# Optimization experiments

Measured on AMD Instinct MI355X. Metric: run time of the kernel, lower is better.

## Reference

```python
import jax, jax.numpy as jnp
import numpy as np

B, T, V, E, H = 4096, 16, 512, 512, 1024


def setup_inputs() -> dict:
    key = jax.random.key(0)
    ks = jax.random.split(key, 8)
    s = 0.05  # weight init scale
    return {
        "encoded_input": jax.random.normal(ks[0], (B, H), jnp.float32),
        "target": jax.random.randint(ks[1], (B, T), 0, V, jnp.int32),
        "emb": jax.random.normal(ks[2], (V, E), jnp.float32) * s,
        "W_ih": jax.random.normal(ks[3], (4 * H, E), jnp.float32) * s,
        "W_hh": jax.random.normal(ks[4], (4 * H, H), jnp.float32) * s,
        "b_ih": jax.random.normal(ks[5], (4 * H,), jnp.float32) * s,
        "b_hh": jax.random.normal(ks[6], (4 * H,), jnp.float32) * s,
        "W_out": jax.random.normal(ks[7], (V, H), jnp.float32) * s,
    }


def reference(encoded_input, target, emb, W_ih, W_hh, b_ih, b_hh, W_out):
    # Teacher-forced char LSTM decoder. Dropout(0.1) is identity in eval mode.
    b, t = target.shape
    # input char ids: start token 0, then shifted targets
    inp_ids = jnp.concatenate(
        [jnp.zeros((b, 1), target.dtype), target[:, :-1]], axis=1)  # [B,T]
    x = emb[inp_ids]  # [B,T,E]
    # precompute input contribution to gates for all steps
    xg = jnp.einsum('bte,ge->btg', x, W_ih) + b_ih + b_hh  # [B,T,4H]

    def step(carry, xs):
        h, c = carry
        xg_t, tgt_t = xs  # [B,4H], [B]
        gates = xg_t + h @ W_hh.T  # [B,4H]
        i, f, g, o = jnp.split(gates, 4, axis=-1)  # torch order i,f,g,o
        i = jax.nn.sigmoid(i)
        f = jax.nn.sigmoid(f)
        g = jnp.tanh(g)
        o = jax.nn.sigmoid(o)
        c = f * c + i * g
        h = o * jnp.tanh(c)
        logits = h @ W_out.T  # [B,V]
        # NLL of log_softmax at target index, expressed stably
        lse = jax.nn.logsumexp(logits, axis=-1)
        tgt_logit = jnp.take_along_axis(logits, tgt_t[:, None], axis=1)[:, 0]
        loss_t = lse - tgt_logit  # [B]
        return (h, c), loss_t

    h0 = encoded_input  # hidden = (encoded, encoded) for 1 layer
    (_, _), losses = jax.lax.scan(
        step, (h0, h0),
        (jnp.swapaxes(xg, 0, 1), target.T))  # scan over time: [T,B,...]
    return losses.sum(axis=0) / t  # [B] per-example mean loss
```

## Files before the change

### kernel.cpp

```cpp
#include <hip/hip_runtime.h>
#include <hip/hip_bf16.h>
#include <stdint.h>

typedef __attribute__((ext_vector_type(8))) short bf16x8;
typedef __attribute__((ext_vector_type(4))) float f32x4;

#define DEV __device__ __forceinline__
#define MFMA16(a, b, c) __builtin_amdgcn_mfma_f32_16x16x32_bf16(a, b, c, 0, 0, 0)

static constexpr int Bn = 4096;
static constexpr int Tn = 16;
static constexpr int Vn = 512;
static constexpr int En = 512;
static constexpr int Hn = 1024;
static constexpr int G4 = 4096;

DEV unsigned short f2bf(float f) {
    union { float f; uint32_t u; } v; v.f = f;
    return (unsigned short)((v.u + 0x7fffu + ((v.u >> 16) & 1u)) >> 16);
}
DEV float bf2f(unsigned short h) {
    union { uint32_t u; float f; } v; v.u = (uint32_t)h << 16; return v.f;
}
DEV float sigmoidf_(float x) { return 1.f / (1.f + __expf(-x)); }
DEV float tanhf_(float x)    { return 1.f - 2.f / (1.f + __expf(2.f * x)); }

DEV bf16x8 cvt8(const float* p) {
    f32x4 a = *(const f32x4*)p;
    f32x4 b = *(const f32x4*)(p + 4);
    bf16x8 o;
    o[0] = (short)f2bf(a[0]); o[1] = (short)f2bf(a[1]);
    o[2] = (short)f2bf(a[2]); o[3] = (short)f2bf(a[3]);
    o[4] = (short)f2bf(b[0]); o[5] = (short)f2bf(b[1]);
    o[6] = (short)f2bf(b[2]); o[7] = (short)f2bf(b[3]);
    return o;
}

#define GLOAD16(s, d) __builtin_amdgcn_global_load_lds( \
    (const __attribute__((address_space(1))) uint32_t*)(s), \
    (__attribute__((address_space(3))) uint32_t*)(d), 16, 0, 0)

__launch_bounds__(512, 2)
__global__ void lstm8(const unsigned short* __restrict__ Whp8,
                      const unsigned short* __restrict__ Hin,
                      const float* __restrict__ EGb,
                      const int* __restrict__ target, int t,
                      float* __restrict__ CstF,
                      unsigned short* __restrict__ Hout)
{
    __shared__ __align__(16) unsigned short lds[65536];

    const int tid = threadIdx.x;
    const int l   = tid & 63;
    const int w   = tid >> 6;
    const int wm  = w >> 2, wn = w & 3;
    const int q   = l >> 4, c15 = l & 15;
    const int bx  = blockIdx.x, by = blockIdx.y;
    const int n0  = bx * 256;

    const int cB    = (((l & 7) ^ (l >> 3)) << 3);
    const int sw0   = ((q ^ (c15 & 7)) << 3);
    const int offA0 = c15 * 64 + sw0;
    const int offB0 = ((wn & 1) * 64 + c15) * 64 + sw0;

    f32x4 acc[8][4];
#pragma unroll
    for (int i = 0; i < 8; i++)
#pragma unroll
        for (int j = 0; j < 4; j++) acc[i][j] = f32x4{0.f, 0.f, 0.f, 0.f};

    auto stA = [&](int kts, int cbuf) {
        const unsigned short* page =
            Whp8 + (((size_t)(by * 16 + kts) * 2) << 13);
#pragma unroll
        for (int h = 0; h < 2; h++)
#pragma unroll
            for (int L = 0; L < 2; L++)
                GLOAD16(page + h * 8192 + L * 4096 + w * 512 + l * 8,
                        &lds[cbuf * 16384 + h * 8192 + L * 4096 + w * 512]);
    };
    auto stB = [&](int kts, int cbuf) {
#pragma unroll
        for (int h = 0; h < 2; h++)
#pragma unroll
            for (int L = 0; L < 2; L++)
                GLOAD16(Hin + (size_t)(n0 + h * 128 + L * 64 + w * 8 + (l >> 3)) * Hn
                            + kts * 64 + cB,
                        &lds[32768 + cbuf * 16384 + h * 8192 + L * 4096 + w * 512]);
    };

    stA(0, 0); stB(0, 0);
    stA(1, 1); stB(1, 1);
    asm volatile("s_waitcnt vmcnt(8)" ::: "memory");
    __builtin_amdgcn_s_barrier();

#pragma unroll 2
    for (int kt = 0; kt < 16; kt++) {
        const int cur = kt & 1;
        const unsigned short* Ab = &lds[cur * 16384 + wm * 8192];
        const unsigned short* Bb = &lds[32768 + cur * 16384 + (wn >> 1) * 8192];
        bf16x8 aF[8], bF[4];

#pragma unroll
        for (int i = 0; i < 8; i++)
            aF[i] = *(const bf16x8*)&Ab[offA0 + i * 1024];
#pragma unroll
        for (int j = 0; j < 4; j++)
            bF[j] = *(const bf16x8*)&Bb[offB0 + j * 1024];
        __builtin_amdgcn_s_setprio(1);
#pragma unroll
        for (int i = 0; i < 8; i++)
#pragma unroll
            for (int j = 0; j < 4; j++)
                acc[i][j] = MFMA16(aF[i], bF[j], acc[i][j]);
        __builtin_amdgcn_s_setprio(0);

#pragma unroll
        for (int i = 0; i < 8; i++)
            aF[i] = *(const bf16x8*)&Ab[(offA0 ^ 32) + i * 1024];
#pragma unroll
        for (int j = 0; j < 4; j++)
            bF[j] = *(const bf16x8*)&Bb[(offB0 ^ 32) + j * 1024];
        __builtin_amdgcn_s_setprio(1);
#pragma unroll
        for (int i = 0; i < 8; i++)
#pragma unroll
            for (int j = 0; j < 4; j++)
                acc[i][j] = MFMA16(aF[i], bF[j], acc[i][j]);
        __builtin_amdgcn_s_setprio(0);
        __builtin_amdgcn_s_barrier();

        const int kts = (kt + 2 < 16) ? (kt + 2) : 15;
        stA(kts, cur);
        stB(kts, cur);
        asm volatile("s_waitcnt vmcnt(8)" ::: "memory");
        __builtin_amdgcn_s_barrier();
    }

    int ids[4];
#pragma unroll
    for (int j = 0; j < 4; j++)
        ids[j] = (t > 0)
            ? target[(size_t)(n0 + wn * 64 + j * 16 + c15) * Tn + (t - 1)] : 0;

    const int U0 = by * 64;
    unsigned short* sH = &lds[32768];
#pragma unroll
    for (int i = 0; i < 8; i++) {
        const int Uloc = wm * 32 + i * 4 + q;
#pragma unroll
        for (int j = 0; j < 4; j++) {
            f32x4 eg = *(const f32x4*)&EGb[(size_t)ids[j] * G4 + (U0 + Uloc) * 4];
            float ig = sigmoidf_(acc[i][j][0] + eg[0]);
            float fg = sigmoidf_(acc[i][j][1] + eg[1]);
            float gg = tanhf_  (acc[i][j][2] + eg[2]);
            float og = sigmoidf_(acc[i][j][3] + eg[3]);
            const size_t cidx =
                ((((size_t)(by * 16 + bx) * 8 + w) * 32 + i * 4 + j) << 6) + l;
            float cOld = CstF[cidx];
            float cNew = fg * cOld + ig * gg;
            float h    = og * tanhf_(cNew);
            CstF[cidx] = cNew;
            const int bl = wn * 64 + j * 16 + c15;
            sH[bl * 64 + (Uloc ^ ((bl & 7) << 3))] = f2bf(h);
        }
    }
    __syncthreads();
    {
        const int row = tid >> 1;
        const int hs  = tid & 1;
        const int sx  = row & 7;
        size_t go = (size_t)(n0 + row) * Hn + U0 + hs * 32;
#pragma unroll
        for (int s = 0; s < 4; s++) {
            const int slog = hs * 4 + s;
            bf16x8 v = *(const bf16x8*)&sH[row * 64 + ((slog ^ sx) << 3)];
            *(bf16x8*)&Hout[go + s * 8] = v;
        }
    }
}

__launch_bounds__(512, 1)
__global__ void logits256(const unsigned short* __restrict__ A,
                          const unsigned short* __restrict__ Wob,
                          const int* __restrict__ target,
                          float* __restrict__ partS,
                          float* __restrict__ partT)
{
    __shared__ __align__(16) unsigned short lds[65536];
    __shared__ float redS[4 * 256];
    __shared__ float redT[4 * 256];
    __shared__ int   tgL[256];

    const int tid = threadIdx.x;
    const int l   = tid & 63;
    const int w   = tid >> 6;
    const int wm  = w >> 2, wn = w & 3;
    const int q   = l >> 4, c15 = l & 15;
    const int bid = blockIdx.x;
    const int rb  = bid & 255, cb = bid >> 8;
    const int r0  = rb * 256;
    const int v0  = cb * 256;

    if (tid < 256) {
        int ra = r0 + tid;
        tgL[tid] = target[(size_t)(ra & (Bn - 1)) * Tn + (ra >> 12)];
    }

    const int cB    = (((l & 7) ^ (l >> 3)) << 3);
    const int sw0   = ((q ^ (c15 & 7)) << 3);
    const int offA0 = c15 * 64 + sw0;
    const int offB0 = ((wn & 1) * 64 + c15) * 64 + sw0;

    f32x4 acc[8][4];
#pragma unroll
    for (int i = 0; i < 8; i++)
#pragma unroll
        for (int j = 0; j < 4; j++) acc[i][j] = f32x4{0.f, 0.f, 0.f, 0.f};

    auto stA = [&](int kts, int cbuf) {
#pragma unroll
        for (int h = 0; h < 2; h++)
#pragma unroll
            for (int L = 0; L < 2; L++)
                GLOAD16(A + (size_t)(r0 + h * 128 + L * 64 + w * 8 + (l >> 3)) * Hn
                            + kts * 64 + cB,
                        &lds[cbuf * 16384 + h * 8192 + L * 4096 + w * 512]);
    };
    auto stB = [&](int kts, int cbuf) {
#pragma unroll
        for (int h = 0; h < 2; h++)
#pragma unroll
            for (int L = 0; L < 2; L++)
                GLOAD16(Wob + (size_t)(v0 + h * 128 + L * 64 + w * 8 + (l >> 3)) * Hn
                            + kts * 64 + cB,
                        &lds[32768 + cbuf * 16384 + h * 8192 + L * 4096 + w * 512]);
    };

    stA(0, 0); stB(0, 0);
    stA(1, 1); stB(1, 1);
    asm volatile("s_waitcnt vmcnt(8)" ::: "memory");
    __builtin_amdgcn_s_barrier();

#pragma unroll 2
    for (int kt = 0; kt < 16; kt++) {
        const int cur = kt & 1;
        const unsigned short* Ab = &lds[cur * 16384 + wm * 8192];
        const unsigned short* Bb = &lds[32768 + cur * 16384 + (wn >> 1) * 8192];
        bf16x8 aF[8], bF[4];

#pragma unroll
        for (int i = 0; i < 8; i++)
            aF[i] = *(const bf16x8*)&Ab[offA0 + i * 1024];
#pragma unroll
        for (int j = 0; j < 4; j++)
            bF[j] = *(const bf16x8*)&Bb[offB0 + j * 1024];
        __builtin_amdgcn_s_setprio(1);
#pragma unroll
        for (int i = 0; i < 8; i++)
#pragma unroll
            for (int j = 0; j < 4; j++)
                acc[i][j] = MFMA16(aF[i], bF[j], acc[i][j]);
        __builtin_amdgcn_s_setprio(0);

#pragma unroll
        for (int i = 0; i < 8; i++)
            aF[i] = *(const bf16x8*)&Ab[(offA0 ^ 32) + i * 1024];
#pragma unroll
        for (int j = 0; j < 4; j++)
            bF[j] = *(const bf16x8*)&Bb[(offB0 ^ 32) + j * 1024];
        __builtin_amdgcn_s_setprio(1);
#pragma unroll
        for (int i = 0; i < 8; i++)
#pragma unroll
            for (int j = 0; j < 4; j++)
                acc[i][j] = MFMA16(aF[i], bF[j], acc[i][j]);
        __builtin_amdgcn_s_setprio(0);
        __builtin_amdgcn_s_barrier();

        const int kts = (kt + 2 < 16) ? (kt + 2) : 15;
        stA(kts, cur);
        stB(kts, cur);
        asm volatile("s_waitcnt vmcnt(8)" ::: "memory");
        __builtin_amdgcn_s_barrier();
    }

#pragma unroll
    for (int i = 0; i < 8; i++)
#pragma unroll
        for (int rr = 0; rr < 4; rr++) {
            const int rloc = wm * 128 + i * 16 + q * 4 + rr;
            const int tg = tgL[rloc];
            float ps = 0.f, tv = 0.f;
#pragma unroll
            for (int j = 0; j < 4; j++) {
                float v = acc[i][j][rr];
                ps += __expf(v);
                int col = v0 + wn * 64 + j * 16 + c15;
                tv += (col == tg) ? v : 0.f;
            }
#pragma unroll
            for (int d = 1; d < 16; d <<= 1) {
                ps += __shfl_xor(ps, d);
                tv += __shfl_xor(tv, d);
            }
            if (c15 == 0) {
                redS[wn * 256 + rloc] = ps;
                redT[wn * 256 + rloc] = tv;
            }
        }
    __syncthreads();
    if (tid < 256) {
        float se = 0.f, tv = 0.f;
#pragma unroll
        for (int k = 0; k < 4; k++) {
            se += redS[k * 256 + tid];
            tv += redT[k * 256 + tid];
        }
        partS[(size_t)cb * (Bn * Tn) + r0 + tid] = se;
        partT[(size_t)cb * (Bn * Tn) + r0 + tid] = tv;
    }
}

template <int BM, int BN, int EPI>
__launch_bounds__(256, 2)
__global__ void gemm_k(const unsigned short* __restrict__ A, int lda,
                       const unsigned short* __restrict__ Bw, int ldb,
                       int K,
                       const float* __restrict__ biasp,
                       float* __restrict__ Out,
                       unsigned short* __restrict__ Outb, int ldo)
{
    constexpr int BK = 32;
    constexpr int WM = BM / 2, WN = BN / 2;
    constexpr int MI = WM / 16, NJ = WN / 16;

    __shared__ __align__(16) unsigned short sA[BM * BK];
    __shared__ __align__(16) unsigned short sB[BN * BK];

    const int tid = threadIdx.x;
    const int l   = tid & 63;
    const int w   = tid >> 6;
    const int wm  = w >> 1, wn = w & 1;
    const int m0  = blockIdx.y * BM;
    const int n0  = blockIdx.x * BN;

    f32x4 acc[MI][NJ];
#pragma unroll
    for (int i = 0; i < MI; i++)
#pragma unroll
        for (int j = 0; j < NJ; j++) acc[i][j] = f32x4{0.f, 0.f, 0.f, 0.f};

    const int srow = l >> 2;
    const int scol = (l & 3) * 8;
    const int q    = l >> 4;
    const int c15  = l & 15;

    for (int k0 = 0; k0 < K; k0 += BK) {
#pragma unroll
        for (int c = 0; c < BM / 64; c++)
            GLOAD16(A + (size_t)(m0 + c * 64 + w * 16 + srow) * lda + k0 + scol,
                    &sA[(c * 64 + w * 16) * BK]);
#pragma unroll
        for (int c = 0; c < BN / 64; c++)
            GLOAD16(Bw + (size_t)(n0 + c * 64 + w * 16 + srow) * ldb + k0 + scol,
                    &sB[(c * 64 + w * 16) * BK]);
        __syncthreads();

        bf16x8 aF[MI], bF[NJ];
#pragma unroll
        for (int i = 0; i < MI; i++)
            aF[i] = *(const bf16x8*)&sA[(wm * WM + i * 16 + c15) * BK + q * 8];
#pragma unroll
        for (int j = 0; j < NJ; j++)
            bF[j] = *(const bf16x8*)&sB[(wn * WN + j * 16 + c15) * BK + q * 8];
#pragma unroll
        for (int i = 0; i < MI; i++)
#pragma unroll
            for (int j = 0; j < NJ; j++)
                acc[i][j] = MFMA16(aF[i], bF[j], acc[i][j]);
        __syncthreads();
    }

#pragma unroll
    for (int j = 0; j < NJ; j++) {
        const int colp = n0 + wn * WN + j * 16 + c15;
        const float bj = biasp ? biasp[colp] : 0.f;
#pragma unroll
        for (int i = 0; i < MI; i++) {
            const size_t rb = (size_t)(m0 + wm * WM + i * 16 + 4 * q);
#pragma unroll
            for (int r = 0; r < 4; r++) {
                float vv = acc[i][j][r] + bj;
                if constexpr (EPI == 0) Out[(rb + r) * ldo + colp] = vv;
                else Outb[(rb + r) * ldo + colp] = f2bf(vv);
            }
        }
    }
}

__global__ void prep_wih(const float* __restrict__ Wih,
                         unsigned short* __restrict__ Wihp)
{
    int i = blockIdx.x * 256 + threadIdx.x;
    int n = i >> 6, kc = (i & 63) * 8;
    int g = n & 3, u = n >> 2;
    *(bf16x8*)&Wihp[(size_t)n * En + kc] =
        cvt8(Wih + (size_t)(g * Hn + u) * En + kc);
}

__global__ void prep_w8(const float* __restrict__ Whh,
                        unsigned short* __restrict__ Whp8)
{
    int idx = blockIdx.x * 256 + threadIdx.x;
    int o = idx * 8;
    int p = o & 8191;
    int h = (o >> 13) & 1;
    int kt = (o >> 14) & 15;
    int by = o >> 18;
    int r = p >> 6;
    int slot = (p & 63) >> 3;
    int cl = ((slot ^ (r & 7)) << 3);
    int n = by * 256 + h * 128 + r;
    int g = n & 3, u = n >> 2;
    *(bf16x8*)&Whp8[o] = cvt8(Whh + (size_t)(g * Hn + u) * Hn + kt * 64 + cl);
}

__global__ void prep_bias(const float* __restrict__ bih,
                          const float* __restrict__ bhh,
                          float* __restrict__ biasp)
{
    int n = blockIdx.x * 256 + threadIdx.x;
    int g = n & 3, u = n >> 2;
    biasp[n] = bih[g * Hn + u] + bhh[g * Hn + u];
}

__global__ void prep_wout(const float* __restrict__ Wout,
                          unsigned short* __restrict__ Wob)
{
    int i = blockIdx.x * 256 + threadIdx.x;
    size_t off = (size_t)i * 8;
    *(bf16x8*)&Wob[off] = cvt8(Wout + off);
}

__global__ void prep_emb(const float* __restrict__ emb,
                         unsigned short* __restrict__ embb)
{
    int i = blockIdx.x * 256 + threadIdx.x;
    size_t off = (size_t)i * 8;
    *(bf16x8*)&embb[off] = cvt8(emb + off);
}

__global__ void init_state(const float* __restrict__ enc,
                           float* __restrict__ CstF,
                           unsigned short* __restrict__ Xh0,
                           float* __restrict__ loss)
{
    int f = blockIdx.x * 256 + threadIdx.x;
    int l = f & 63, q = l >> 4, c15 = l & 15;
    int ij = (f >> 6) & 31, i = ij >> 2, j = ij & 3;
    int w = (f >> 11) & 7, wm = w >> 2, wn = w & 3;
    int bx = (f >> 14) & 15, by = (f >> 18) & 15;
    int b = bx * 256 + wn * 64 + j * 16 + c15;
    int U = by * 64 + wm * 32 + i * 4 + q;
    CstF[f] = enc[(size_t)b * Hn + U];
    if (f < Bn * Hn / 8) {
        int m = f >> 7, u8 = (f & 127) * 8;
        *(bf16x8*)&Xh0[(size_t)m * Hn + u8] = cvt8(enc + (size_t)m * Hn + u8);
    }
    if (f < Bn) loss[f] = 0.f;
}

__global__ void lse_k(const unsigned short* __restrict__ lg,
                      const int* __restrict__ target, int t,
                      float* __restrict__ lossOut)
{
    int w = threadIdx.x >> 6, l = threadIdx.x & 63;
    int ra = blockIdx.x * 4 + w;
    const unsigned short* row = lg + (size_t)ra * Vn;
    bf16x8 v = *(const bf16x8*)&row[l * 8];
    float x0 = bf2f((unsigned short)v[0]), x1 = bf2f((unsigned short)v[1]);
    float x2 = bf2f((unsigned short)v[2]), x3 = bf2f((unsigned short)v[3]);
    float x4 = bf2f((unsigned short)v[4]), x5 = bf2f((unsigned short)v[5]);
    float x6 = bf2f((unsigned short)v[6]), x7 = bf2f((unsigned short)v[7]);
    float mx = fmaxf(fmaxf(fmaxf(x0, x1), fmaxf(x2, x3)),
                     fmaxf(fmaxf(x4, x5), fmaxf(x6, x7)));
#pragma unroll
    for (int d = 1; d < 64; d <<= 1) mx = fmaxf(mx, __shfl_xor(mx, d));
    float se = __expf(x0 - mx) + __expf(x1 - mx) + __expf(x2 - mx) +
               __expf(x3 - mx) + __expf(x4 - mx) + __expf(x5 - mx) +
               __expf(x6 - mx) + __expf(x7 - mx);
#pragma unroll
    for (int d = 1; d < 64; d <<= 1) se += __shfl_xor(se, d);
    if (l == 0) {
        int tg = target[(size_t)ra * Tn + t];
        lossOut[ra] += (mx + __logf(se)) - bf2f(row[tg]);
    }
}

__global__ void finalize_p(const float* __restrict__ partS,
                           const float* __restrict__ partT,
                           float* __restrict__ out)
{
    int m = blockIdx.x * 256 + threadIdx.x;
    float s = 0.f;
#pragma unroll
    for (int k = 0; k < 16; k++) {
        size_t ra = (size_t)k * Bn + m;
        float se = partS[ra] + partS[(size_t)(Bn * Tn) + ra];
        float tv = partT[ra] + partT[(size_t)(Bn * Tn) + ra];
        s += __logf(se) - tv;
    }
    out[m] = s * (1.f / 16.f);
}

__global__ void finalize_s(const float* __restrict__ loss,
                           float* __restrict__ out)
{
    int m = blockIdx.x * 256 + threadIdx.x;
    out[m] = loss[m] * (1.f / 16.f);
}

extern "C" void kernel_launch(void* const* d_in, const int* in_sizes, int n_in,
                              void* d_out, int out_size, void* d_ws, size_t ws_size,
                              hipStream_t stream)
{
    const float* enc    = (const float*)d_in[0];
    const int*   target = (const int*)d_in[1];
    const float* emb    = (const float*)d_in[2];
    const float* Wih    = (const float*)d_in[3];
    const float* Whh    = (const float*)d_in[4];
    const float* bih    = (const float*)d_in[5];
    const float* bhh    = (const float*)d_in[6];
    const float* Wout   = (const float*)d_in[7];
    float* out = (float*)d_out;
    (void)in_sizes; (void)n_in; (void)out_size;

    constexpr size_t SZ_Wihp  = (size_t)G4 * En * 2;
    constexpr size_t SZ_Whp8  = (size_t)G4 * Hn * 2;
    constexpr size_t SZ_Wob   = (size_t)Vn * Hn * 2;
    constexpr size_t SZ_biasp = (size_t)G4 * 4;
    constexpr size_t SZ_embb  = (size_t)Vn * En * 2;
    constexpr size_t SZ_EGb   = (size_t)Vn * G4 * 4;
    constexpr size_t SZ_Cst   = (size_t)Bn * Hn * 4;
    constexpr size_t SZ_H     = (size_t)Bn * Hn * 2;
    constexpr size_t SZ_LGS   = (size_t)Bn * Vn * 2;
    constexpr size_t SZ_PART  = (size_t)2 * Bn * Tn * 4;
    auto pad = [](size_t b) { return (b + 255) & ~(size_t)255; };
    const size_t fixed = pad(SZ_Wihp) + pad(SZ_Whp8) + pad(SZ_Wob) +
                         pad(SZ_biasp) + pad(SZ_embb) + pad(SZ_EGb) +
                         pad(SZ_Cst);
    const size_t needB = fixed + 17 * pad(SZ_H) + pad(SZ_LGS) +
                         2 * pad(SZ_PART);
    const bool batched = ws_size >= needB;

    size_t off = 0;
    char* base = (char*)d_ws;
    auto alloc = [&](size_t bytes) -> void* {
        void* p = base + off; off += pad(bytes); return p;
    };
    unsigned short* Wihp  = (unsigned short*)alloc(SZ_Wihp);
    unsigned short* Whp8  = (unsigned short*)alloc(SZ_Whp8);
    unsigned short* Wob   = (unsigned short*)alloc(SZ_Wob);
    float*          biasp = (float*)alloc(SZ_biasp);
    unsigned short* embb  = (unsigned short*)alloc(SZ_embb);
    float*          EGb   = (float*)alloc(SZ_EGb);
    float*          CstF  = (float*)alloc(SZ_Cst);
    const int nslot = batched ? 17 : 3;
    unsigned short* Hs    = (unsigned short*)alloc((size_t)nslot * pad(SZ_H));
    unsigned short* lgS   = (unsigned short*)alloc(SZ_LGS);
    float*          partS = (float*)alloc(SZ_PART);
    float*          partT = (float*)alloc(SZ_PART);
    const size_t HSLOT = pad(SZ_H) / 2;

    prep_wih  <<<1024, 256, 0, stream>>>(Wih, Wihp);
    prep_w8   <<<2048, 256, 0, stream>>>(Whh, Whp8);
    prep_bias <<<16,   256, 0, stream>>>(bih, bhh, biasp);
    prep_wout <<<256,  256, 0, stream>>>(Wout, Wob);
    prep_emb  <<<128,  256, 0, stream>>>(emb, embb);
    init_state<<<16384, 256, 0, stream>>>(enc, CstF, Hs, partS);

    gemm_k<128, 128, 0><<<dim3(32, 4), 256, 0, stream>>>(
        embb, En, Wihp, En, En, biasp, EGb, nullptr, G4);

    if (batched) {
        for (int t = 0; t < Tn; t++)
            lstm8<<<dim3(16, 16), 512, 0, stream>>>(
                Whp8, Hs + (size_t)t * HSLOT, EGb, target, t, CstF,
                Hs + (size_t)(t + 1) * HSLOT);
        logits256<<<512, 512, 0, stream>>>(
            Hs + HSLOT, Wob, target, partS, partT);
        finalize_p<<<16, 256, 0, stream>>>(partS, partT, out);
    } else {
        for (int t = 0; t < Tn; t++) {
            unsigned short* hIn  = Hs + (size_t)(t % 3) * HSLOT;
            unsigned short* hOut = Hs + (size_t)((t + 1) % 3) * HSLOT;
            lstm8<<<dim3(16, 16), 512, 0, stream>>>(
                Whp8, hIn, EGb, target, t, CstF, hOut);
            gemm_k<128, 64, 2><<<dim3(8, 32), 256, 0, stream>>>(
                hOut, Hn, Wob, Hn, Hn, nullptr, nullptr, lgS, Vn);
            lse_k<<<1024, 256, 0, stream>>>(lgS, target, t, partS);
        }
        finalize_s<<<16, 256, 0, stream>>>(partS, out);
    }
}
```

Before: 883.1 us.

## Store gate-input table in bf16 and prefetch it with cell state before GEMM

```diff
diff --git a/kernel.cpp b/kernel.cpp
--- a/kernel.cpp
+++ b/kernel.cpp
@@ -43,7 +43,7 @@
 __launch_bounds__(512, 2)
 __global__ void lstm8(const unsigned short* __restrict__ Whp8,
                       const unsigned short* __restrict__ Hin,
-                      const float* __restrict__ EGb,
+                      const unsigned short* __restrict__ EGb,
                       const int* __restrict__ target, int t,
                       float* __restrict__ CstF,
                       unsigned short* __restrict__ Hout)
@@ -57,11 +57,36 @@
     const int q   = l >> 4, c15 = l & 15;
     const int bx  = blockIdx.x, by = blockIdx.y;
     const int n0  = bx * 256;
+    const int U0  = by * 64;
 
     const int cB    = (((l & 7) ^ (l >> 3)) << 3);
     const int sw0   = ((q ^ (c15 & 7)) << 3);
     const int offA0 = c15 * 64 + sw0;
     const int offB0 = ((wn & 1) * 64 + c15) * 64 + sw0;
+
+    int ids[4];
+#pragma unroll
+    for (int j = 0; j < 4; j++)
+        ids[j] = (t > 0)
+            ? target[(size_t)(n0 + wn * 64 + j * 16 + c15) * Tn + (t - 1)] : 0;
+    uint2 egPre[8][4];
+#pragma unroll
+    for (int i = 0; i < 8; i++) {
+        const int Uloc = wm * 32 + i * 4 + q;
+#pragma unroll
+        for (int j = 0; j < 4; j++)
+            egPre[i][j] =
+                *(const uint2*)&EGb[(size_t)ids[j] * G4 + (U0 + Uloc) * 4];
+    }
+    float cPre[8][4];
+#pragma unroll
+    for (int i = 0; i < 8; i++)
+#pragma unroll
+        for (int j = 0; j < 4; j++) {
+            const size_t cidx =
+                ((((size_t)(by * 16 + bx) * 8 + w) * 32 + i * 4 + j) << 6) + l;
+            cPre[i][j] = CstF[cidx];
+        }
 
     f32x4 acc[8][4];
 #pragma unroll
@@ -137,28 +162,24 @@
         __builtin_amdgcn_s_barrier();
     }
 
-    int ids[4];
-#pragma unroll
-    for (int j = 0; j < 4; j++)
-        ids[j] = (t > 0)
-            ? target[(size_t)(n0 + wn * 64 + j * 16 + c15) * Tn + (t - 1)] : 0;
-
-    const int U0 = by * 64;
     unsigned short* sH = &lds[32768];
 #pragma unroll
     for (int i = 0; i < 8; i++) {
         const int Uloc = wm * 32 + i * 4 + q;
 #pragma unroll
         for (int j = 0; j < 4; j++) {
-            f32x4 eg = *(const f32x4*)&EGb[(size_t)ids[j] * G4 + (U0 + Uloc) * 4];
-            float ig = sigmoidf_(acc[i][j][0] + eg[0]);
-            float fg = sigmoidf_(acc[i][j][1] + eg[1]);
-            float gg = tanhf_  (acc[i][j][2] + eg[2]);
-            float og = sigmoidf_(acc[i][j][3] + eg[3]);
+            uint2 egu = egPre[i][j];
+            float e0 = bf2f((unsigned short)(egu.x & 0xffffu));
+            float e1 = bf2f((unsigned short)(egu.x >> 16));
+            float e2 = bf2f((unsigned short)(egu.y & 0xffffu));
+            float e3 = bf2f((unsigned short)(egu.y >> 16));
+            float ig = sigmoidf_(acc[i][j][0] + e0);
+            float fg = sigmoidf_(acc[i][j][1] + e1);
+            float gg = tanhf_  (acc[i][j][2] + e2);
+            float og = sigmoidf_(acc[i][j][3] + e3);
             const size_t cidx =
                 ((((size_t)(by * 16 + bx) * 8 + w) * 32 + i * 4 + j) << 6) + l;
-            float cOld = CstF[cidx];
-            float cNew = fg * cOld + ig * gg;
+            float cNew = fg * cPre[i][j] + ig * gg;
             float h    = og * tanhf_(cNew);
             CstF[cidx] = cNew;
             const int bl = wn * 64 + j * 16 + c15;
@@ -541,7 +562,7 @@
     constexpr size_t SZ_Wob   = (size_t)Vn * Hn * 2;
     constexpr size_t SZ_biasp = (size_t)G4 * 4;
     constexpr size_t SZ_embb  = (size_t)Vn * En * 2;
-    constexpr size_t SZ_EGb   = (size_t)Vn * G4 * 4;
+    constexpr size_t SZ_EGb   = (size_t)Vn * G4 * 2;
     constexpr size_t SZ_Cst   = (size_t)Bn * Hn * 4;
     constexpr size_t SZ_H     = (size_t)Bn * Hn * 2;
     constexpr size_t SZ_LGS   = (size_t)Bn * Vn * 2;
@@ -564,7 +585,7 @@
     unsigned short* Wob   = (unsigned short*)alloc(SZ_Wob);
     float*          biasp = (float*)alloc(SZ_biasp);
     unsigned short* embb  = (unsigned short*)alloc(SZ_embb);
-    float*          EGb   = (float*)alloc(SZ_EGb);
+    unsigned short* EGb   = (unsigned short*)alloc(SZ_EGb);
     float*          CstF  = (float*)alloc(SZ_Cst);
     const int nslot = batched ? 17 : 3;
     unsigned short* Hs    = (unsigned short*)alloc((size_t)nslot * pad(SZ_H));
@@ -580,8 +601,8 @@
     prep_emb  <<<128,  256, 0, stream>>>(emb, embb);
     init_state<<<16384, 256, 0, stream>>>(enc, CstF, Hs, partS);
 
-    gemm_k<128, 128, 0><<<dim3(32, 4), 256, 0, stream>>>(
-        embb, En, Wihp, En, En, biasp, EGb, nullptr, G4);
+    gemm_k<128, 128, 2><<<dim3(32, 4), 256, 0, stream>>>(
+        embb, En, Wihp, En, En, biasp, nullptr, EGb, G4);
 
     if (batched) {
         for (int t = 0; t < Tn; t++)
```

After: 1.290 ms. 1.46x slower.
